# Optimization experiments

Measured on AMD Instinct MI355X. Metric: run time of the kernel, lower is better.

## Reference

```python
import math
import jax, jax.numpy as jnp
import numpy as np

B, T, C = 8, 4096, 1024
N_HEAD = 16
HS = C // N_HEAD  # head_size = 64


def _keep_indices(T):
    # Faithful Python/math replication of the row-gather index list.
    a = math.ceil(T / 4)
    keep = [T - 1 - x for x in range(a)]
    keep += [T - 1 - math.ceil(3 / a * (x - a) ** 2 + a) for x in range(a, math.ceil(T / 2))]
    return np.array(list(reversed(keep)), dtype=np.int32)  # [K] = [ceil(T/2)]


def setup_inputs() -> dict:
    key = jax.random.key(0)
    ks = jax.random.split(key, 7)
    s = 1.0 / math.sqrt(C)  # torch Linear default init scale
    return {
        "x": jax.random.normal(ks[0], (B, T, C), dtype=jnp.float32),
        "Wq": jax.random.uniform(ks[1], (HS, C), jnp.float32, -s, s),
        "bq": jax.random.uniform(ks[2], (HS,), jnp.float32, -s, s),
        "Wk": jax.random.uniform(ks[3], (HS, C), jnp.float32, -s, s),
        "bk": jax.random.uniform(ks[4], (HS,), jnp.float32, -s, s),
        "Wv": jax.random.uniform(ks[5], (HS, C), jnp.float32, -s, s),
        "bv": jax.random.uniform(ks[6], (HS,), jnp.float32, -s, s),
    }


def reference(x, Wq, bq, Wk, bk, Wv, bv):
    Bx, Tx, Cx = x.shape
    keep = jnp.asarray(_keep_indices(Tx))                    # [K], static
    q = x @ Wq.T + bq                                        # [B,T,hs]
    k = x @ Wk.T + bk                                        # [B,T,hs]
    v = x @ Wv.T + bv                                        # [B,T,hs]
    # Original computes full q@k^T then gathers rows; gathering q rows first
    # is the same math without materializing [B,T,T].
    qg = q[:, keep, :]                                       # [B,K,hs]
    att = jnp.einsum('bkd,btd->bkt', qg, k) * (Cx ** -0.5)   # scale by n_embd, per source
    # fade_tril = tril[keep, :T]: row i allows positions j <= keep[i]
    mask = jnp.arange(Tx)[None, :] <= keep[:, None]          # [K,T]
    att = jnp.where(mask[None], att, -jnp.inf)
    att = jax.nn.softmax(att, axis=-1)
    # dropout p=0.0 -> identity
    out = jnp.einsum('bkt,btd->bkd', att, v)                 # [B,K,hs]
    return out
```

## Files before the change

kernel.cpp:

```cpp
#include <hip/hip_runtime.h>
#include <hip/hip_bf16.h>

typedef __attribute__((ext_vector_type(8))) short s8v;
typedef __attribute__((ext_vector_type(4))) short s4v;
typedef __attribute__((ext_vector_type(4))) float f4v;

#define B_   8
#define T_   4096
#define C_   1024
#define HS_  64
#define K2_  2048

__device__ __forceinline__ int keep_of(int i) {
    if (i >= 1024) return 2048 + i;
    int d = 1023 - i;
    return 3071 - ((3 * d * d + 1023) >> 10);
}

__device__ __forceinline__ short bf16_bits(float f) {
    union { __hip_bfloat16 h; short s; } u;
    u.h = __float2bfloat16(f);
    return u.s;
}

__device__ __forceinline__ s8v cvt8f(const float* p) {
    const f4v a = *(const f4v*)p;
    const f4v b = *(const f4v*)(p + 4);
    s8v r;
    r[0] = bf16_bits(a[0]); r[1] = bf16_bits(a[1]);
    r[2] = bf16_bits(a[2]); r[3] = bf16_bits(a[3]);
    r[4] = bf16_bits(b[0]); r[5] = bf16_bits(b[1]);
    r[6] = bf16_bits(b[2]); r[7] = bf16_bits(b[3]);
    return r;
}

__device__ __forceinline__ void gload_lds16(const void* g, void* l) {
    __builtin_amdgcn_global_load_lds(
        (__attribute__((address_space(1))) void*)(g),
        (__attribute__((address_space(3))) void*)(l), 16, 0, 0);
}

__global__ __launch_bounds__(256) void wcvt_kernel(
    const float* __restrict__ Wq, const float* __restrict__ Wk,
    const float* __restrict__ Wv, short* __restrict__ Wb)
{
    const int idx = (blockIdx.x * 256 + threadIdx.x) * 8;
    const int mat = idx >> 16;
    const int off = idx & 65535;
    const float* src = (mat == 0) ? Wq : (mat == 1) ? Wk : Wv;
    *(s8v*)(Wb + idx) = cvt8f(src + off);
}

__global__ __launch_bounds__(256) void qkv_kernel(
    const float* __restrict__ x,
    const short* __restrict__ Wb,
    const float* __restrict__ bq, const float* __restrict__ bk,
    const float* __restrict__ bv,
    __hip_bfloat16* __restrict__ Qo, __hip_bfloat16* __restrict__ Ko,
    __hip_bfloat16* __restrict__ Vt)
{
    __shared__ __align__(16) char smem[40960];
    float* xs  = (float*)smem;
    short* wsm = (short*)(smem + 16384);

    const int tid  = threadIdx.x;
    const int wave = tid >> 6;
    const int lane = tid & 63;
    const int l16  = lane & 15;
    const int quad = lane >> 4;
    const int row0 = blockIdx.x * 64;

    f4v acc[3][4];
    #pragma unroll
    for (int m = 0; m < 3; ++m)
        #pragma unroll
        for (int mt = 0; mt < 4; ++mt) {
            acc[m][mt][0] = 0.f; acc[m][mt][1] = 0.f;
            acc[m][mt][2] = 0.f; acc[m][mt][3] = 0.f;
        }

    int xrow[4], xoff[4];
    #pragma unroll
    for (int i = 0; i < 4; ++i) {
        const int f = 256 * i + tid;
        xrow[i] = f >> 4;
        xoff[i] = ((f & 15) ^ (xrow[i] & 7)) * 4;
    }
    int wrow[6], woff[6];
    #pragma unroll
    for (int i = 0; i < 6; ++i) {
        const int f = 256 * i + tid;
        wrow[i] = f >> 3;
        woff[i] = ((f & 7) ^ (wrow[i] & 7)) * 8;
    }

    for (int k0 = 0; k0 < C_; k0 += 64) {
        __syncthreads();
        #pragma unroll
        for (int i = 0; i < 4; ++i)
            gload_lds16(x + (size_t)(row0 + xrow[i]) * C_ + k0 + xoff[i],
                        (char*)xs + (256 * i + tid) * 16);
        #pragma unroll
        for (int i = 0; i < 6; ++i)
            gload_lds16(Wb + (size_t)wrow[i] * C_ + k0 + woff[i],
                        (char*)wsm + (256 * i + tid) * 16);
        __syncthreads();

        #pragma unroll
        for (int kh = 0; kh < 2; ++kh) {
            s8v a[4];
            #pragma unroll
            for (int mt = 0; mt < 4; ++mt) {
                const int r   = mt * 16 + l16;
                const int ch0 = kh * 8 + quad * 2;
                const float* p0 = xs + r * 64 + ((ch0    ) ^ (r & 7)) * 4;
                const float* p1 = xs + r * 64 + ((ch0 + 1) ^ (r & 7)) * 4;
                const f4v u = *(const f4v*)p0;
                const f4v v = *(const f4v*)p1;
                s8v af;
                af[0] = bf16_bits(u[0]); af[1] = bf16_bits(u[1]);
                af[2] = bf16_bits(u[2]); af[3] = bf16_bits(u[3]);
                af[4] = bf16_bits(v[0]); af[5] = bf16_bits(v[1]);
                af[6] = bf16_bits(v[2]); af[7] = bf16_bits(v[3]);
                a[mt] = af;
            }
            #pragma unroll
            for (int m = 0; m < 3; ++m) {
                const int wr = m * 64 + wave * 16 + l16;
                const int ch = kh * 4 + quad;
                const s8v bf = *(const s8v*)(wsm + wr * 64 + ((ch ^ (wr & 7)) * 8));
                #pragma unroll
                for (int mt = 0; mt < 4; ++mt)
                    acc[m][mt] = __builtin_amdgcn_mfma_f32_16x16x32_bf16(a[mt], bf, acc[m][mt], 0, 0, 0);
            }
        }
    }

    const int wc = wave * 16 + l16;
    const float bqv = bq[wc], bkv = bk[wc], bvv = bv[wc];
    #pragma unroll
    for (int mt = 0; mt < 4; ++mt) {
        const int rbase = row0 + mt * 16 + quad * 4;
        #pragma unroll
        for (int r = 0; r < 4; ++r) {
            Qo[(size_t)(rbase + r) * HS_ + wc] = __float2bfloat16(acc[0][mt][r] + bqv);
            Ko[(size_t)(rbase + r) * HS_ + wc] = __float2bfloat16(acc[1][mt][r] + bkv);
        }
        s4v vp;
        #pragma unroll
        for (int r = 0; r < 4; ++r) vp[r] = bf16_bits(acc[2][mt][r] + bvv);
        const int bb = rbase >> 12;
        const int tt = rbase & (T_ - 1);
        *(s4v*)(Vt + ((size_t)(bb * HS_ + wc)) * T_ + tt) = vp;
    }
}

__global__ __launch_bounds__(256) void attn_kernel(
    const __hip_bfloat16* __restrict__ Qo,
    const __hip_bfloat16* __restrict__ Ko,
    const __hip_bfloat16* __restrict__ Vt,
    float* __restrict__ out)
{
    __shared__ __align__(16) char smem[17408];
    float* mL = (float*)smem;
    float* mO = (float*)(smem + 256);

    const int b    = blockIdx.x & 7;
    const int pp   = blockIdx.x >> 3;
    const int tid  = threadIdx.x;
    const int wave = tid >> 6;
    const int lane = tid & 63;
    const int l16  = lane & 15;
    const int quad = lane >> 4;

    short* pw0 = (short*)smem + wave * 2048;

    const __hip_bfloat16* kbase = Ko + (size_t)b * T_ * HS_;
    const __hip_bfloat16* vbase = Vt + (size_t)b * HS_ * T_;

    #pragma unroll 1
    for (int which = 0; which < 2; ++which) {
        const int qb = which ? (63 - pp) : (64 + pp);

        const int qt = keep_of(qb * 16 + l16);
        const __hip_bfloat16* qrow = Qo + ((size_t)(b * T_ + qt)) * HS_;
        const s8v aq0 = *(const s8v*)(qrow + quad * 8);
        const s8v aq1 = *(const s8v*)(qrow + 32 + quad * 8);

        int keepr[4];
        #pragma unroll
        for (int r = 0; r < 4; ++r) keepr[r] = keep_of(qb * 16 + quad * 4 + r);

        const int kmin   = keep_of(qb * 16);
        const int tmax   = keep_of(qb * 16 + 15);
        const int ntiles = (tmax >> 6) + 1;

        f4v accO[4];
        #pragma unroll
        for (int j = 0; j < 4; ++j) { accO[j][0]=0.f; accO[j][1]=0.f; accO[j][2]=0.f; accO[j][3]=0.f; }
        float l_p[4] = {0.f, 0.f, 0.f, 0.f};

        s8v kreg[8], vreg[8];

        int tt = wave;
        if (tt < ntiles) {
            const int t0 = tt << 6;
            #pragma unroll
            for (int jn = 0; jn < 4; ++jn) {
                const __hip_bfloat16* kr = kbase + (size_t)(t0 + jn * 16 + l16) * HS_ + quad * 8;
                kreg[jn * 2    ] = *(const s8v*)(kr);
                kreg[jn * 2 + 1] = *(const s8v*)(kr + 32);
            }
            #pragma unroll
            for (int jd = 0; jd < 4; ++jd) {
                const __hip_bfloat16* vr = vbase + (size_t)(jd * 16 + l16) * T_ + t0 + quad * 8;
                vreg[jd * 2    ] = *(const s8v*)(vr);
                vreg[jd * 2 + 1] = *(const s8v*)(vr + 32);
            }
        }

        for (; tt < ntiles; tt += 4) {
            const int t0 = tt << 6;
            const int tn = tt + 4;
            short* pw = pw0 + ((tt >> 2) & 1) * 1024;

            f4v s4[4];
            #pragma unroll
            for (int jn = 0; jn < 4; ++jn) {
                f4v z; z[0]=0.f; z[1]=0.f; z[2]=0.f; z[3]=0.f;
                z = __builtin_amdgcn_mfma_f32_16x16x32_bf16(aq0, kreg[jn * 2    ], z, 0, 0, 0);
                z = __builtin_amdgcn_mfma_f32_16x16x32_bf16(aq1, kreg[jn * 2 + 1], z, 0, 0, 0);
                s4[jn] = z;
            }

            if (tn < ntiles) {
                const int t0n = tn << 6;
                #pragma unroll
                for (int jn = 0; jn < 4; ++jn) {
                    const __hip_bfloat16* kr = kbase + (size_t)(t0n + jn * 16 + l16) * HS_ + quad * 8;
                    kreg[jn * 2    ] = *(const s8v*)(kr);
                    kreg[jn * 2 + 1] = *(const s8v*)(kr + 32);
                }
            }

            if (t0 + 63 <= kmin) {
                #pragma unroll
                for (int jn = 0; jn < 4; ++jn) {
                    const int t = jn * 16 + l16;
                    const int chunk = t >> 3;
                    #pragma unroll
                    for (int r = 0; r < 4; ++r) {
                        const float p = __expf(s4[jn][r] * 0.03125f);
                        l_p[r] += p;
                        const int m = quad * 4 + r;
                        pw[m * 64 + ((chunk ^ (m & 7)) * 8) + (t & 7)] = bf16_bits(p);
                    }
                }
            } else {
                #pragma unroll
                for (int jn = 0; jn < 4; ++jn) {
                    const int t = jn * 16 + l16;
                    const int valid_t = t0 + t;
                    const int chunk = t >> 3;
                    #pragma unroll
                    for (int r = 0; r < 4; ++r) {
                        const float e = __expf(s4[jn][r] * 0.03125f);
                        const float p = (valid_t <= keepr[r]) ? e : 0.0f;
                        l_p[r] += p;
                        const int m = quad * 4 + r;
                        pw[m * 64 + ((chunk ^ (m & 7)) * 8) + (t & 7)] = bf16_bits(p);
                    }
                }
            }
            const s8v ap0 = *(const s8v*)(pw + l16 * 64 + ((quad    ) ^ (l16 & 7)) * 8);
            const s8v ap1 = *(const s8v*)(pw + l16 * 64 + ((quad + 4) ^ (l16 & 7)) * 8);

            #pragma unroll
            for (int jd = 0; jd < 4; ++jd) {
                accO[jd] = __builtin_amdgcn_mfma_f32_16x16x32_bf16(ap0, vreg[jd * 2    ], accO[jd], 0, 0, 0);
                accO[jd] = __builtin_amdgcn_mfma_f32_16x16x32_bf16(ap1, vreg[jd * 2 + 1], accO[jd], 0, 0, 0);
            }

            if (tn < ntiles) {
                const int t0n = tn << 6;
                #pragma unroll
                for (int jd = 0; jd < 4; ++jd) {
                    const __hip_bfloat16* vr = vbase + (size_t)(jd * 16 + l16) * T_ + t0n + quad * 8;
                    vreg[jd * 2    ] = *(const s8v*)(vr);
                    vreg[jd * 2 + 1] = *(const s8v*)(vr + 32);
                }
            }
        }

        #pragma unroll
        for (int off = 1; off < 16; off <<= 1)
            #pragma unroll
            for (int r = 0; r < 4; ++r) l_p[r] += __shfl_xor(l_p[r], off);

        __syncthreads();
        #pragma unroll
        for (int r = 0; r < 4; ++r) {
            const int row = quad * 4 + r;
            if (l16 == 0) mL[wave * 16 + row] = l_p[r];
            #pragma unroll
            for (int jd = 0; jd < 4; ++jd)
                mO[wave * 1024 + row * 64 + jd * 16 + l16] = accO[jd][r];
        }
        __syncthreads();

        {
            const int row = tid >> 4;
            const int col = (tid & 15) * 4;
            float L = 0.f;
            #pragma unroll
            for (int w = 0; w < 4; ++w) L += mL[w * 16 + row];
            const float inv = 1.0f / L;
            f4v o; o[0]=0.f; o[1]=0.f; o[2]=0.f; o[3]=0.f;
            #pragma unroll
            for (int w = 0; w < 4; ++w) {
                const f4v ow = *(const f4v*)(mO + w * 1024 + row * 64 + col);
                #pragma unroll
                for (int j = 0; j < 4; ++j) o[j] += ow[j];
            }
            #pragma unroll
            for (int j = 0; j < 4; ++j) o[j] *= inv;
            *(f4v*)(out + ((size_t)(b * K2_ + qb * 16 + row)) * HS_ + col) = o;
        }
        __syncthreads();
    }
}

extern "C" void kernel_launch(void* const* d_in, const int* in_sizes, int n_in,
                              void* d_out, int out_size, void* d_ws, size_t ws_size,
                              hipStream_t stream) {
    (void)in_sizes; (void)n_in; (void)out_size; (void)ws_size;
    const float* x  = (const float*)d_in[0];
    const float* Wq = (const float*)d_in[1];
    const float* bq = (const float*)d_in[2];
    const float* Wk = (const float*)d_in[3];
    const float* bk = (const float*)d_in[4];
    const float* Wv = (const float*)d_in[5];
    const float* bv = (const float*)d_in[6];

    __hip_bfloat16* Qo = (__hip_bfloat16*)d_ws;
    __hip_bfloat16* Ko = Qo + (size_t)B_ * T_ * HS_;
    __hip_bfloat16* Vt = Ko + (size_t)B_ * T_ * HS_;
    short*          Wb = (short*)(Vt + (size_t)B_ * HS_ * T_);
    float* o = (float*)d_out;

    wcvt_kernel<<<dim3(96), dim3(256), 0, stream>>>(Wq, Wk, Wv, Wb);
    qkv_kernel<<<dim3((B_ * T_) / 64), dim3(256), 0, stream>>>(
        x, Wb, bq, bk, bv, Qo, Ko, Vt);
    attn_kernel<<<dim3(512), dim3(256), 0, stream>>>(Qo, Ko, Vt, o);
}
```

Before: 295.7 us.

## Stage K/V tiles in LDS via direct global-to-LDS loads with tiled V layout

The projection kernel now writes V in a 64-token tiled layout, so each 64x64 V tile is contiguous in memory. The attention kernel replaces per-wave register prefetch of K and V with block-cooperative direct global-to-LDS loads into swizzled shared buffers, followed by MFMA operand reads from LDS. The aim is fully coalesced, asynchronous tile transfers. In exchange it drops the register double-buffered prefetch, adds two block barriers per step, and raises LDS use to 72KB, which lowers occupancy. Each wave still consumes only its own tile, so staging gives no data reuse across waves.

```diff
diff --git a/kernel.cpp b/kernel.cpp
--- a/kernel.cpp
+++ b/kernel.cpp
@@ -150,8 +150,9 @@
         #pragma unroll
         for (int r = 0; r < 4; ++r) vp[r] = bf16_bits(acc[2][mt][r] + bvv);
         const int bb = rbase >> 12;
-        const int tt = rbase & (T_ - 1);
-        *(s4v*)(Vt + ((size_t)(bb * HS_ + wc)) * T_ + tt) = vp;
+        const int t  = rbase & (T_ - 1);
+        *(s4v*)(Vt + (size_t)bb * HS_ * T_
+                   + (size_t)(t & ~63) * HS_ + wc * 64 + (t & 63)) = vp;
     }
 }
 
@@ -161,7 +162,9 @@
     const __hip_bfloat16* __restrict__ Vt,
     float* __restrict__ out)
 {
-    __shared__ __align__(16) char smem[17408];
+    __shared__ __align__(16) char smem[73728];
+    short* Ks = (short*)smem;
+    short* Vs = (short*)(smem + 32768);
     float* mL = (float*)smem;
     float* mO = (float*)(smem + 256);
 
@@ -173,10 +176,21 @@
     const int l16  = lane & 15;
     const int quad = lane >> 4;
 
-    short* pw0 = (short*)smem + wave * 2048;
-
-    const __hip_bfloat16* kbase = Ko + (size_t)b * T_ * HS_;
-    const __hip_bfloat16* vbase = Vt + (size_t)b * HS_ * T_;
+    short* pw = (short*)(smem + 65536) + wave * 1024;
+
+    const short* kb = (const short*)Ko + (size_t)b * T_ * HS_;
+    const short* vb = (const short*)Vt + (size_t)b * HS_ * T_;
+
+    int kgoff[8], vgoff[8];
+    #pragma unroll
+    for (int j = 0; j < 8; ++j) {
+        const int ki = j * 256 + tid;
+        const int kr = ki >> 3;
+        kgoff[j] = kr * 64 + (((tid & 7) ^ (kr & 7)) * 8);
+        const int vs_ = ki >> 9;
+        const int vd  = (ki & 511) >> 3;
+        vgoff[j] = (vs_ * 64 + vd) * 64 + (((tid & 7) ^ (vd & 7)) * 8);
+    }
 
     #pragma unroll 1
     for (int which = 0; which < 2; ++which) {
@@ -194,100 +208,80 @@
         const int kmin   = keep_of(qb * 16);
         const int tmax   = keep_of(qb * 16 + 15);
         const int ntiles = (tmax >> 6) + 1;
+        const int nsteps = (ntiles + 3) >> 2;
 
         f4v accO[4];
         #pragma unroll
         for (int j = 0; j < 4; ++j) { accO[j][0]=0.f; accO[j][1]=0.f; accO[j][2]=0.f; accO[j][3]=0.f; }
         float l_p[4] = {0.f, 0.f, 0.f, 0.f};
 
-        s8v kreg[8], vreg[8];
-
-        int tt = wave;
-        if (tt < ntiles) {
-            const int t0 = tt << 6;
-            #pragma unroll
-            for (int jn = 0; jn < 4; ++jn) {
-                const __hip_bfloat16* kr = kbase + (size_t)(t0 + jn * 16 + l16) * HS_ + quad * 8;
-                kreg[jn * 2    ] = *(const s8v*)(kr);
-                kreg[jn * 2 + 1] = *(const s8v*)(kr + 32);
-            }
-            #pragma unroll
-            for (int jd = 0; jd < 4; ++jd) {
-                const __hip_bfloat16* vr = vbase + (size_t)(jd * 16 + l16) * T_ + t0 + quad * 8;
-                vreg[jd * 2    ] = *(const s8v*)(vr);
-                vreg[jd * 2 + 1] = *(const s8v*)(vr + 32);
-            }
-        }
-
-        for (; tt < ntiles; tt += 4) {
-            const int t0 = tt << 6;
-            const int tn = tt + 4;
-            short* pw = pw0 + ((tt >> 2) & 1) * 1024;
-
-            f4v s4[4];
-            #pragma unroll
-            for (int jn = 0; jn < 4; ++jn) {
-                f4v z; z[0]=0.f; z[1]=0.f; z[2]=0.f; z[3]=0.f;
-                z = __builtin_amdgcn_mfma_f32_16x16x32_bf16(aq0, kreg[jn * 2    ], z, 0, 0, 0);
-                z = __builtin_amdgcn_mfma_f32_16x16x32_bf16(aq1, kreg[jn * 2 + 1], z, 0, 0, 0);
-                s4[jn] = z;
-            }
-
-            if (tn < ntiles) {
-                const int t0n = tn << 6;
+        for (int s = 0; s < nsteps; ++s) {
+            const int t064 = s << 14;
+
+            __syncthreads();
+            #pragma unroll
+            for (int j = 0; j < 8; ++j)
+                gload_lds16(kb + t064 + kgoff[j], (char*)smem + (j * 256 + tid) * 16);
+            #pragma unroll
+            for (int j = 0; j < 8; ++j)
+                gload_lds16(vb + t064 + vgoff[j], (char*)smem + 32768 + (j * 256 + tid) * 16);
+            __syncthreads();
+
+            const int ttg = s * 4 + wave;
+            if (ttg < ntiles) {
+                const int t0 = ttg << 6;
+
+                f4v s4[4];
                 #pragma unroll
                 for (int jn = 0; jn < 4; ++jn) {
-                    const __hip_bfloat16* kr = kbase + (size_t)(t0n + jn * 16 + l16) * HS_ + quad * 8;
-                    kreg[jn * 2    ] = *(const s8v*)(kr);
-                    kreg[jn * 2 + 1] = *(const s8v*)(kr + 32);
+                    const int row = wave * 64 + jn * 16 + l16;
+                    const s8v bk0 = *(const s8v*)(Ks + row * 64 + (((quad    ) ^ (row & 7)) * 8));
+                    const s8v bk1 = *(const s8v*)(Ks + row * 64 + (((quad + 4) ^ (row & 7)) * 8));
+                    f4v z; z[0]=0.f; z[1]=0.f; z[2]=0.f; z[3]=0.f;
+                    z = __builtin_amdgcn_mfma_f32_16x16x32_bf16(aq0, bk0, z, 0, 0, 0);
+                    z = __builtin_amdgcn_mfma_f32_16x16x32_bf16(aq1, bk1, z, 0, 0, 0);
+                    s4[jn] = z;
                 }
-            }
-
-            if (t0 + 63 <= kmin) {
-                #pragma unroll
-                for (int jn = 0; jn < 4; ++jn) {
-                    const int t = jn * 16 + l16;
-                    const int chunk = t >> 3;
+
+                if (t0 + 63 <= kmin) {
                     #pragma unroll
-                    for (int r = 0; r < 4; ++r) {
-                        const float p = __expf(s4[jn][r] * 0.03125f);
-                        l_p[r] += p;
-                        const int m = quad * 4 + r;
-                        pw[m * 64 + ((chunk ^ (m & 7)) * 8) + (t & 7)] = bf16_bits(p);
+                    for (int jn = 0; jn < 4; ++jn) {
+                        const int t = jn * 16 + l16;
+                        const int chunk = t >> 3;
+                        #pragma unroll
+                        for (int r = 0; r < 4; ++r) {
+                            const float p = __expf(s4[jn][r] * 0.03125f);
+                            l_p[r] += p;
+                            const int m = quad * 4 + r;
+                            pw[m * 64 + ((chunk ^ (m & 7)) * 8) + (t & 7)] = bf16_bits(p);
+                        }
+                    }
+                } else {
+                    #pragma unroll
+                    for (int jn = 0; jn < 4; ++jn) {
+                        const int t = jn * 16 + l16;
+                        const int valid_t = t0 + t;
+                        const int chunk = t >> 3;
+                        #pragma unroll
+                        for (int r = 0; r < 4; ++r) {
+                            const float e = __expf(s4[jn][r] * 0.03125f);
+                            const float p = (valid_t <= keepr[r]) ? e : 0.0f;
+                            l_p[r] += p;
+                            const int m = quad * 4 + r;
+                            pw[m * 64 + ((chunk ^ (m & 7)) * 8) + (t & 7)] = bf16_bits(p);
+                        }
                     }
                 }
-            } else {
-                #pragma unroll
-                for (int jn = 0; jn < 4; ++jn) {
-                    const int t = jn * 16 + l16;
-                    const int valid_t = t0 + t;
-                    const int chunk = t >> 3;
-                    #pragma unroll
-                    for (int r = 0; r < 4; ++r) {
-                        const float e = __expf(s4[jn][r] * 0.03125f);
-                        const float p = (valid_t <= keepr[r]) ? e : 0.0f;
-                        l_p[r] += p;
-                        const int m = quad * 4 + r;
-                        pw[m * 64 + ((chunk ^ (m & 7)) * 8) + (t & 7)] = bf16_bits(p);
-                    }
-                }
-            }
-            const s8v ap0 = *(const s8v*)(pw + l16 * 64 + ((quad    ) ^ (l16 & 7)) * 8);
-            const s8v ap1 = *(const s8v*)(pw + l16 * 64 + ((quad + 4) ^ (l16 & 7)) * 8);
-
-            #pragma unroll
-            for (int jd = 0; jd < 4; ++jd) {
-                accO[jd] = __builtin_amdgcn_mfma_f32_16x16x32_bf16(ap0, vreg[jd * 2    ], accO[jd], 0, 0, 0);
-                accO[jd] = __builtin_amdgcn_mfma_f32_16x16x32_bf16(ap1, vreg[jd * 2 + 1], accO[jd], 0, 0, 0);
-            }
-
-            if (tn < ntiles) {
-                const int t0n = tn << 6;
+                const s8v ap0 = *(const s8v*)(pw + l16 * 64 + ((quad    ) ^ (l16 & 7)) * 8);
+                const s8v ap1 = *(const s8v*)(pw + l16 * 64 + ((quad + 4) ^ (l16 & 7)) * 8);
+
                 #pragma unroll
                 for (int jd = 0; jd < 4; ++jd) {
-                    const __hip_bfloat16* vr = vbase + (size_t)(jd * 16 + l16) * T_ + t0n + quad * 8;
-                    vreg[jd * 2    ] = *(const s8v*)(vr);
-                    vreg[jd * 2 + 1] = *(const s8v*)(vr + 32);
+                    const int rd = jd * 16 + l16;
+                    const s8v bv0 = *(const s8v*)(Vs + wave * 4096 + rd * 64 + (((quad    ) ^ (rd & 7)) * 8));
+                    const s8v bv1 = *(const s8v*)(Vs + wave * 4096 + rd * 64 + (((quad + 4) ^ (rd & 7)) * 8));
+                    accO[jd] = __builtin_amdgcn_mfma_f32_16x16x32_bf16(ap0, bv0, accO[jd], 0, 0, 0);
+                    accO[jd] = __builtin_amdgcn_mfma_f32_16x16x32_bf16(ap1, bv1, accO[jd], 0, 0, 0);
                 }
             }
         }
```

After: 252.6 us. -14.6%, faster.
